# Kernel tuning notes

Hardware: AMD Instinct MI355X
Metric: run time of the kernel (lower is better)

## Reference

```python
import jax, jax.numpy as jnp
import numpy as np

B, S, E, H = 2, 2048, 2048, 16
D = E // H  # head_dim = 128
ROPE_BASE = 10000.0


def _rope_tables(seq_len, dim, dtype):
    inv_freq = 1.0 / (ROPE_BASE ** (jnp.arange(0, dim, 2, dtype=jnp.float32) / dim))
    pos = jnp.arange(seq_len, dtype=jnp.float32)
    freqs = jnp.outer(pos, inv_freq)            # [S, D/2]
    emb = jnp.concatenate([freqs, freqs], -1)    # [S, D]
    return jnp.cos(emb).astype(dtype), jnp.sin(emb).astype(dtype)


def _rotate_half(x):
    x1, x2 = jnp.split(x, 2, axis=-1)
    return jnp.concatenate([-x2, x1], axis=-1)


def _apply_rope(x, cos, sin):
    # x: [B,H,S,D]; cos/sin: [S,D] broadcast over batch+heads
    return x * cos[None, None] + _rotate_half(x) * sin[None, None]


def setup_inputs() -> dict:
    key = jax.random.key(0)
    k1, k2, k3 = jax.random.split(key, 3)
    x = jax.random.normal(k1, (B, S, E), dtype=jnp.float32)
    w_qkv = jax.random.normal(k2, (3 * E, E), dtype=jnp.float32) * (E ** -0.5)
    w_out = jax.random.normal(k3, (E, E), dtype=jnp.float32) * (E ** -0.5)
    return {"x": x, "w_qkv": w_qkv, "w_out": w_out}


def reference(x, w_qkv, w_out):
    b, s, e = x.shape
    qkv = x @ w_qkv.T                                # [B,S,3E]
    q, k, v = jnp.split(qkv, 3, axis=-1)
    def to_heads(t):
        return t.reshape(b, s, H, D).transpose(0, 2, 1, 3)  # [B,H,S,D]
    q, k, v = to_heads(q), to_heads(k), to_heads(v)
    cos, sin = _rope_tables(s, D, x.dtype)
    q = _apply_rope(q, cos, sin)
    k = _apply_rope(k, cos, sin)
    scale = 1.0 / jnp.sqrt(jnp.asarray(D, x.dtype))
    scores = jnp.einsum('bhqd,bhkd->bhqk', q, k) * scale
    causal = jnp.tril(jnp.ones((s, s), dtype=bool))
    scores = jnp.where(causal[None, None], scores, jnp.asarray(-jnp.inf, scores.dtype))
    attn = jax.nn.softmax(scores, axis=-1)
    y = jnp.einsum('bhqk,bhkd->bhqd', attn, v)       # [B,H,S,D]
    y = y.transpose(0, 2, 1, 3).reshape(b, s, e)
    return y @ w_out.T
```

## Files before the change

### kernel.cpp

```cpp
#include <hip/hip_runtime.h>
#include <stdint.h>

constexpr int BATCH = 2;
constexpr int SEQ   = 2048;
constexpr int EMB   = 2048;
constexpr int NH    = 16;
constexpr int HD    = 128;
constexpr int QKV3  = 3 * EMB;

typedef unsigned short u16;
typedef __attribute__((ext_vector_type(8))) short bf16x8;
typedef __attribute__((ext_vector_type(4))) float floatx4;

__device__ inline float bf2f(u16 u) {
  union { unsigned int i; float f; } v; v.i = ((unsigned int)u) << 16; return v.f;
}
__device__ inline u16 f2bf(float f) {
  union { float f; unsigned int i; } v; v.f = f;
  unsigned int x = v.i;
  return (u16)((x + 0x7fffu + ((x >> 16) & 1u)) >> 16);
}

__device__ inline void load_lds16(const void* g, void* l) {
  __builtin_amdgcn_global_load_lds((const __attribute__((address_space(1))) unsigned int*)g,
                                   (__attribute__((address_space(3))) unsigned int*)l,
                                   16, 0, 0);
}

__device__ inline void block_barrier() {
  __builtin_amdgcn_sched_barrier(0);
  asm volatile("" ::: "memory");
  __builtin_amdgcn_s_barrier();
  asm volatile("" ::: "memory");
  __builtin_amdgcn_sched_barrier(0);
}

__global__ void cvt_f32_bf16(const float* __restrict__ src, u16* __restrict__ dst, int n4) {
  const int i = blockIdx.x * blockDim.x + threadIdx.x;
  if (i < n4) {
    const float4 v = ((const float4*)src)[i];
    ushort4 o;
    o.x = f2bf(v.x); o.y = f2bf(v.y); o.z = f2bf(v.z); o.w = f2bf(v.w);
    ((ushort4*)dst)[i] = o;
  }
}

__global__ __launch_bounds__(512, 2) void gemm_bt192(const u16* __restrict__ A,
                                                     const u16* __restrict__ Bm,
                                                     u16* __restrict__ Cb,
                                                     int M, int N, int K) {
  __shared__ __align__(16) u16 sh[57344];
  char* ldsb = (char*)sh;

  const int tid  = threadIdx.x;
  const int wave = tid >> 6, lane = tid & 63;
  const int wrow = wave >> 1;
  const int wcol = wave & 1;
  const int m0 = blockIdx.y * 256, n0 = blockIdx.x * 192;
  const int frow = lane & 15, quad = lane >> 4;
  const int KT = K >> 6;

  const int srow8 = tid >> 3;
  const int scolE = (((tid & 7) ^ (srow8 & 7)) << 3);
  auto stage1 = [&](int t, int d, int j) {
    if (j < 4) {
      const int r = j * 64 + srow8;
      load_lds16(A + (size_t)(m0 + r) * K + t * 64 + scolE,
                 ldsb + d * 57344 + j * 8192 + wave * 1024);
    } else {
      const int bi = j - 4;
      const int r = bi * 64 + srow8;
      load_lds16(Bm + (size_t)(n0 + r) * K + t * 64 + scolE,
                 ldsb + d * 57344 + 32768 + bi * 8192 + wave * 1024);
    }
  };

  floatx4 acc[4][6];
#pragma unroll
  for (int i = 0; i < 4; ++i)
#pragma unroll
    for (int j = 0; j < 6; ++j) acc[i][j] = {0.f, 0.f, 0.f, 0.f};

#pragma unroll
  for (int j = 0; j < 7; ++j) stage1(0, 0, j);

  auto rdA = [&](const char* dbuf, int mi, int kk) -> bf16x8 {
    const int ra = wrow * 64 + mi * 16 + frow;
    const int cb = (kk * 64 + quad * 16) ^ ((ra & 7) << 4);
    return *(const bf16x8*)(dbuf + ra * 128 + cb);
  };
  auto rdB = [&](const char* dbuf, int ni, int kk) -> bf16x8 {
    const int rb = wcol * 96 + ni * 16 + frow;
    const int cb = (kk * 64 + quad * 16) ^ ((rb & 7) << 4);
    return *(const bf16x8*)(dbuf + 32768 + rb * 128 + cb);
  };

  for (int t = 0; t < KT; ++t) {
    const int d = t & 1, dn = d ^ 1;
    const char* dbuf = ldsb + d * 57344;
    const bool pf = (t + 1 < KT);

    asm volatile("s_waitcnt vmcnt(0)" ::: "memory");
    block_barrier();

    bf16x8 a0[2][2], a1[2][2], b0[3][2], b1[3][2];

#pragma unroll
    for (int mi = 0; mi < 2; ++mi)
#pragma unroll
      for (int kk = 0; kk < 2; ++kk) a0[mi][kk] = rdA(dbuf, mi, kk);
#pragma unroll
    for (int ni = 0; ni < 3; ++ni)
#pragma unroll
      for (int kk = 0; kk < 2; ++kk) b0[ni][kk] = rdB(dbuf, ni, kk);
    if (pf) { stage1(t + 1, dn, 0); stage1(t + 1, dn, 1); stage1(t + 1, dn, 2); }
    block_barrier();
    asm volatile("s_waitcnt lgkmcnt(0)" ::: "memory");
    __builtin_amdgcn_sched_barrier(0);
    __builtin_amdgcn_s_setprio(1);
#pragma unroll
    for (int mi = 0; mi < 2; ++mi)
#pragma unroll
      for (int ni = 0; ni < 3; ++ni)
#pragma unroll
        for (int kk = 0; kk < 2; ++kk)
          acc[mi][ni] = __builtin_amdgcn_mfma_f32_16x16x32_bf16(a0[mi][kk], b0[ni][kk], acc[mi][ni], 0, 0, 0);
    __builtin_amdgcn_s_setprio(0);
    block_barrier();

#pragma unroll
    for (int mi = 0; mi < 2; ++mi)
#pragma unroll
      for (int kk = 0; kk < 2; ++kk) a1[mi][kk] = rdA(dbuf, 2 + mi, kk);
    if (pf) { stage1(t + 1, dn, 3); stage1(t + 1, dn, 4); }
    block_barrier();
    asm volatile("s_waitcnt lgkmcnt(0)" ::: "memory");
    __builtin_amdgcn_sched_barrier(0);
    __builtin_amdgcn_s_setprio(1);
#pragma unroll
    for (int mi = 0; mi < 2; ++mi)
#pragma unroll
      for (int ni = 0; ni < 3; ++ni)
#pragma unroll
        for (int kk = 0; kk < 2; ++kk)
          acc[2 + mi][ni] = __builtin_amdgcn_mfma_f32_16x16x32_bf16(a1[mi][kk], b0[ni][kk], acc[2 + mi][ni], 0, 0, 0);
    __builtin_amdgcn_s_setprio(0);
    block_barrier();

#pragma unroll
    for (int ni = 0; ni < 3; ++ni)
#pragma unroll
      for (int kk = 0; kk < 2; ++kk) b1[ni][kk] = rdB(dbuf, 3 + ni, kk);
    if (pf) { stage1(t + 1, dn, 5); stage1(t + 1, dn, 6); }
    block_barrier();
    asm volatile("s_waitcnt lgkmcnt(0)" ::: "memory");
    __builtin_amdgcn_sched_barrier(0);
    __builtin_amdgcn_s_setprio(1);
#pragma unroll
    for (int mi = 0; mi < 2; ++mi)
#pragma unroll
      for (int ni = 0; ni < 3; ++ni)
#pragma unroll
        for (int kk = 0; kk < 2; ++kk)
          acc[2 + mi][3 + ni] = __builtin_amdgcn_mfma_f32_16x16x32_bf16(a1[mi][kk], b1[ni][kk], acc[2 + mi][3 + ni], 0, 0, 0);
    __builtin_amdgcn_s_setprio(0);
    block_barrier();

    __builtin_amdgcn_s_setprio(1);
#pragma unroll
    for (int mi = 0; mi < 2; ++mi)
#pragma unroll
      for (int ni = 0; ni < 3; ++ni)
#pragma unroll
        for (int kk = 0; kk < 2; ++kk)
          acc[mi][3 + ni] = __builtin_amdgcn_mfma_f32_16x16x32_bf16(a0[mi][kk], b1[ni][kk], acc[mi][3 + ni], 0, 0, 0);
    __builtin_amdgcn_s_setprio(0);
    block_barrier();
  }

#pragma unroll
  for (int mi = 0; mi < 4; ++mi)
#pragma unroll
    for (int ni = 0; ni < 6; ++ni) {
      const int row = m0 + wrow * 64 + mi * 16 + quad * 4;
      const int col = n0 + wcol * 96 + ni * 16 + frow;
#pragma unroll
      for (int r = 0; r < 4; ++r)
        Cb[(size_t)(row + r) * N + col] = f2bf(acc[mi][ni][r]);
    }
}

__global__ __launch_bounds__(512, 2) void gemm_bt128f(const u16* __restrict__ A,
                                                      const u16* __restrict__ Bm,
                                                      float* __restrict__ Cf,
                                                      int M, int N, int K) {
  __shared__ __align__(16) u16 sh[49152];
  char* ldsb = (char*)sh;

  const int tid  = threadIdx.x;
  const int wave = tid >> 6, lane = tid & 63;
  const int wrow = wave >> 1;
  const int wcol = wave & 1;
  const int m0 = blockIdx.y * 256, n0 = blockIdx.x * 128;
  const int frow = lane & 15, quad = lane >> 4;
  const int KT = K >> 6;

  const int srow8 = tid >> 3;
  const int scolE = (((tid & 7) ^ (srow8 & 7)) << 3);
  auto stage1 = [&](int t, int d, int j) {
    if (j < 4) {
      const int r = j * 64 + srow8;
      load_lds16(A + (size_t)(m0 + r) * K + t * 64 + scolE,
                 ldsb + d * 49152 + j * 8192 + wave * 1024);
    } else {
      const int bi = j - 4;
      const int r = bi * 64 + srow8;
      load_lds16(Bm + (size_t)(n0 + r) * K + t * 64 + scolE,
                 ldsb + d * 49152 + 32768 + bi * 8192 + wave * 1024);
    }
  };

  floatx4 acc[4][4];
#pragma unroll
  for (int i = 0; i < 4; ++i)
#pragma unroll
    for (int j = 0; j < 4; ++j) acc[i][j] = {0.f, 0.f, 0.f, 0.f};

#pragma unroll
  for (int j = 0; j < 6; ++j) stage1(0, 0, j);

  auto rdA = [&](const char* dbuf, int mi, int kk) -> bf16x8 {
    const int ra = wrow * 64 + mi * 16 + frow;
    const int cb = (kk * 64 + quad * 16) ^ ((ra & 7) << 4);
    return *(const bf16x8*)(dbuf + ra * 128 + cb);
  };
  auto rdB = [&](const char* dbuf, int ni, int kk) -> bf16x8 {
    const int rb = wcol * 64 + ni * 16 + frow;
    const int cb = (kk * 64 + quad * 16) ^ ((rb & 7) << 4);
    return *(const bf16x8*)(dbuf + 32768 + rb * 128 + cb);
  };

  for (int t = 0; t < KT; ++t) {
    const int d = t & 1, dn = d ^ 1;
    const char* dbuf = ldsb + d * 49152;
    const bool pf = (t + 1 < KT);

    asm volatile("s_waitcnt vmcnt(0)" ::: "memory");
    block_barrier();

    bf16x8 af[4][2], b0[2][2], b1[2][2];

#pragma unroll
    for (int mi = 0; mi < 4; ++mi)
#pragma unroll
      for (int kk = 0; kk < 2; ++kk) af[mi][kk] = rdA(dbuf, mi, kk);
#pragma unroll
    for (int ni = 0; ni < 2; ++ni)
#pragma unroll
      for (int kk = 0; kk < 2; ++kk) b0[ni][kk] = rdB(dbuf, ni, kk);
    if (pf) { stage1(t + 1, dn, 0); stage1(t + 1, dn, 1); stage1(t + 1, dn, 2); }
    block_barrier();
    asm volatile("s_waitcnt lgkmcnt(0)" ::: "memory");
    __builtin_amdgcn_sched_barrier(0);
    __builtin_amdgcn_s_setprio(1);
#pragma unroll
    for (int mi = 0; mi < 4; ++mi)
#pragma unroll
      for (int ni = 0; ni < 2; ++ni)
#pragma unroll
        for (int kk = 0; kk < 2; ++kk)
          acc[mi][ni] = __builtin_amdgcn_mfma_f32_16x16x32_bf16(af[mi][kk], b0[ni][kk], acc[mi][ni], 0, 0, 0);
    __builtin_amdgcn_s_setprio(0);
    block_barrier();

#pragma unroll
    for (int ni = 0; ni < 2; ++ni)
#pragma unroll
      for (int kk = 0; kk < 2; ++kk) b1[ni][kk] = rdB(dbuf, 2 + ni, kk);
    if (pf) { stage1(t + 1, dn, 3); stage1(t + 1, dn, 4); stage1(t + 1, dn, 5); }
    block_barrier();
    asm volatile("s_waitcnt lgkmcnt(0)" ::: "memory");
    __builtin_amdgcn_sched_barrier(0);
    __builtin_amdgcn_s_setprio(1);
#pragma unroll
    for (int mi = 0; mi < 4; ++mi)
#pragma unroll
      for (int ni = 0; ni < 2; ++ni)
#pragma unroll
        for (int kk = 0; kk < 2; ++kk)
          acc[mi][2 + ni] = __builtin_amdgcn_mfma_f32_16x16x32_bf16(af[mi][kk], b1[ni][kk], acc[mi][2 + ni], 0, 0, 0);
    __builtin_amdgcn_s_setprio(0);
    block_barrier();
  }

#pragma unroll
  for (int mi = 0; mi < 4; ++mi)
#pragma unroll
    for (int ni = 0; ni < 4; ++ni) {
      const int row = m0 + wrow * 64 + mi * 16 + quad * 4;
      const int col = n0 + wcol * 64 + ni * 16 + frow;
#pragma unroll
      for (int r = 0; r < 4; ++r)
        Cf[(size_t)(row + r) * N + col] = acc[mi][ni][r];
    }
}

__global__ void rope_inplace(u16* __restrict__ qkv) {
  const int t   = blockIdx.x * blockDim.x + threadIdx.x;
  const int j   = t & 63;
  const int idx = t >> 6;
  const int h   = idx & (NH - 1);
  const int bs  = idx >> 4;
  const int s   = bs & (SEQ - 1);

  u16* base = qkv + (size_t)bs * QKV3 + h * HD;

  const float inv_freq = exp2f(-(float)j * (13.287712379549449f / 64.0f));
  const float ang = (float)s * inv_freq;
  const float c = cosf(ang), sn = sinf(ang);

#pragma unroll
  for (int part = 0; part < 2; ++part) {
    u16* p = base + part * EMB;
    const float x1 = bf2f(p[j]), x2 = bf2f(p[j + 64]);
    p[j]      = f2bf(x1 * c - x2 * sn);
    p[j + 64] = f2bf(x2 * c + x1 * sn);
  }
}

__global__ __launch_bounds__(256) void transpose_v(const u16* __restrict__ qkv,
                                                   u16* __restrict__ VT) {
  __shared__ u16 vtile[64][136];
  const int tid = threadIdx.x;
  const int s0 = blockIdx.x * 64;
  const int bh = blockIdx.y;
  const int b = bh >> 4, h = bh & 15;

  const u16* Vp = qkv + (size_t)b * SEQ * QKV3 + 2 * EMB + h * HD;
  {
    const int r = tid >> 2, cp = (tid & 3) * 32;
    const uint4* src = (const uint4*)(Vp + (size_t)(s0 + r) * QKV3 + cp);
    uint4* dst = (uint4*)&vtile[r][cp];
    dst[0] = src[0]; dst[1] = src[1]; dst[2] = src[2]; dst[3] = src[3];
  }
  __syncthreads();
  {
    const int d = tid >> 1, ck = (tid & 1) * 32;
    ushort4 o[8];
#pragma unroll
    for (int i = 0; i < 8; ++i) {
      o[i].x = vtile[ck + i * 4 + 0][d];
      o[i].y = vtile[ck + i * 4 + 1][d];
      o[i].z = vtile[ck + i * 4 + 2][d];
      o[i].w = vtile[ck + i * 4 + 3][d];
    }
    ushort4* dst = (ushort4*)(VT + ((size_t)bh * HD + d) * SEQ + s0 + ck);
#pragma unroll
    for (int i = 0; i < 8; ++i) dst[i] = o[i];
  }
}

constexpr int PSTR = 72;

__global__ __launch_bounds__(256, 2) void attn_mfma(const u16* __restrict__ qkv,
                                                    const u16* __restrict__ VT,
                                                    u16* __restrict__ Y) {
  __shared__ __align__(16) u16 kb[2][64 * 128];
  __shared__ __align__(16) u16 vb[2][64 * 128];
  __shared__ __align__(16) u16 p_sh[4][16][PSTR];

  const int tid  = threadIdx.x;
  const int wave = tid >> 6, lane = tid & 63;
  const int bid  = blockIdx.x;
  const int bh   = bid & 31;
  const int pc   = bid >> 5;
  const int cq   = (pc < 8) ? pc : 23 - pc;
  const int qa   = cq;
  const int qb   = 31 - cq;
  const int b = bh >> 4, h = bh & 15;

  const u16* Qp  = qkv + (size_t)b * SEQ * QKV3 + h * HD;
  const u16* Kp  = Qp + EMB;
  const u16* VTp = VT + (size_t)bh * HD * SEQ;

  const int NT = 32 - cq;

  u16* kbf = &kb[0][0];

  {
    const int rl  = lane >> 4;
    const int cbp = (lane & 15) * 16;
#pragma unroll
    for (int i = 0; i < 8; ++i) {
      const int cc = wave * 8 + i;
      const int r  = cc * 4 + rl;
      const int gq = (r < 64) ? (qa * 64 + r) : (qb * 64 + r - 64);
      const int cbl = cbp ^ ((r & 7) << 4);
      load_lds16(Qp + (size_t)gq * QKV3 + (cbl >> 1), kbf + cc * 512);
    }
  }
  asm volatile("s_waitcnt vmcnt(0)" ::: "memory");
  block_barrier();

  const int frow = lane & 15;
  const int quad = lane >> 4;

  bf16x8 aq[2][4];
#pragma unroll
  for (int m = 0; m < 2; ++m)
#pragma unroll
    for (int ks = 0; ks < 4; ++ks) {
      const int qr = m * 64 + wave * 16 + frow;
      const int cb = (ks * 64 + quad * 16) ^ ((qr & 7) << 4);
      aq[m][ks] = *(const bf16x8*)((const char*)kbf + qr * 256 + cb);
    }
  asm volatile("s_waitcnt lgkmcnt(0)" ::: "memory");
  block_barrier();

  auto stage_k = [&](int t, int sel) {
    const int rl  = lane >> 4;
    const int cbp = (lane & 15) * 16;
#pragma unroll
    for (int i = 0; i < 4; ++i) {
      const int cc = wave * 4 + i;
      const int r  = cc * 4 + rl;
      const int cbl = cbp ^ ((r & 7) << 4);
      load_lds16(Kp + (size_t)(t * 64 + r) * QKV3 + (cbl >> 1), &kb[sel][cc * 512]);
    }
  };
  auto stage_v = [&](int t, int sel) {
    const int rl  = lane >> 3;
    const int cbp = (lane & 7) * 16;
#pragma unroll
    for (int i = 0; i < 4; ++i) {
      const int cc = wave * 4 + i;
      const int r  = cc * 8 + rl;
      const int cbl = cbp ^ ((r & 7) << 4);
      load_lds16(VTp + (size_t)r * SEQ + t * 64 + (cbl >> 1), &vb[sel][cc * 512]);
    }
  };

  floatx4 o_acc[2][8];
#pragma unroll
  for (int m = 0; m < 2; ++m)
#pragma unroll
    for (int dt = 0; dt < 8; ++dt) o_acc[m][dt] = {0.f, 0.f, 0.f, 0.f};
  float l_r[2][4];
#pragma unroll
  for (int m = 0; m < 2; ++m)
#pragma unroll
    for (int r = 0; r < 4; ++r) l_r[m][r] = 0.f;

  const float scale = 0.08838834764831845f;
  const float M0s   = 3.5355339059327378f;

  stage_k(0, 0);
  stage_v(0, 0);

  for (int t = 0; t < NT; ++t) {
    block_barrier();
    const bool havek = (t + 1 < NT);
    if (havek) {
      stage_k(t + 1, (t + 1) & 1);
      stage_v(t + 1, (t + 1) & 1);
      asm volatile("s_waitcnt vmcnt(8)" ::: "memory");
    } else {
      asm volatile("s_waitcnt vmcnt(0)" ::: "memory");
    }
    block_barrier();

    const char* kbuf = (const char*)&kb[t & 1][0];
    const char* vbuf = (const char*)&vb[t & 1][0];
    const bool aAct = (t <= qa);

    floatx4 s4[2][4];
    __builtin_amdgcn_s_setprio(1);
    if (aAct) {
#pragma unroll
      for (int nt = 0; nt < 4; ++nt) {
        floatx4 a0 = {0.f, 0.f, 0.f, 0.f}, a1 = {0.f, 0.f, 0.f, 0.f};
#pragma unroll
        for (int ks = 0; ks < 4; ++ks) {
          const int kr = nt * 16 + frow;
          const int cb = (ks * 64 + quad * 16) ^ ((kr & 7) << 4);
          const bf16x8 bk = *(const bf16x8*)(kbuf + kr * 256 + cb);
          a0 = __builtin_amdgcn_mfma_f32_16x16x32_bf16(aq[0][ks], bk, a0, 0, 0, 0);
          a1 = __builtin_amdgcn_mfma_f32_16x16x32_bf16(aq[1][ks], bk, a1, 0, 0, 0);
        }
        s4[0][nt] = a0; s4[1][nt] = a1;
      }
    } else {
#pragma unroll
      for (int nt = 0; nt < 4; ++nt) {
        floatx4 a1 = {0.f, 0.f, 0.f, 0.f};
#pragma unroll
        for (int ks = 0; ks < 4; ++ks) {
          const int kr = nt * 16 + frow;
          const int cb = (ks * 64 + quad * 16) ^ ((kr & 7) << 4);
          const bf16x8 bk = *(const bf16x8*)(kbuf + kr * 256 + cb);
          a1 = __builtin_amdgcn_mfma_f32_16x16x32_bf16(aq[1][ks], bk, a1, 0, 0, 0);
        }
        s4[1][nt] = a1;
      }
    }
    __builtin_amdgcn_s_setprio(0);

#pragma unroll
    for (int m = 0; m < 2; ++m) {
      if (m == 0 && !aAct) continue;
      const int tdiag = (m == 0) ? qa : qb;
      if (t == tdiag) {
#pragma unroll
        for (int nt = 0; nt < 4; ++nt)
#pragma unroll
          for (int r = 0; r < 4; ++r) {
            const int key = t * 64 + nt * 16 + frow;
            const int qg  = tdiag * 64 + wave * 16 + quad * 4 + r;
            if (key > qg) s4[m][nt][r] = -1.0e30f;
          }
      }
#pragma unroll
      for (int nt = 0; nt < 4; ++nt)
#pragma unroll
        for (int r = 0; r < 4; ++r)
          s4[m][nt][r] = __expf(fmaf(s4[m][nt][r], scale, -M0s));
#pragma unroll
      for (int r = 0; r < 4; ++r)
        l_r[m][r] += (s4[m][0][r] + s4[m][1][r]) + (s4[m][2][r] + s4[m][3][r]);
    }

    __builtin_amdgcn_s_setprio(1);
#pragma unroll
    for (int m = 0; m < 2; ++m) {
      if (m == 0 && !aAct) continue;
#pragma unroll
      for (int nt = 0; nt < 4; ++nt)
#pragma unroll
        for (int r = 0; r < 4; ++r)
          p_sh[wave][quad * 4 + r][nt * 16 + frow] = f2bf(s4[m][nt][r]);
#pragma unroll
      for (int step = 0; step < 2; ++step) {
        const bf16x8 ap = *(const bf16x8*)&p_sh[wave][frow][step * 32 + quad * 8];
#pragma unroll
        for (int dt = 0; dt < 8; ++dt) {
          const int vr = dt * 16 + frow;
          const int cb = (step * 64 + quad * 16) ^ ((vr & 7) << 4);
          const bf16x8 bv = *(const bf16x8*)(vbuf + vr * 128 + cb);
          o_acc[m][dt] = __builtin_amdgcn_mfma_f32_16x16x32_bf16(ap, bv, o_acc[m][dt], 0, 0, 0);
        }
      }
    }
    __builtin_amdgcn_s_setprio(0);
  }

#pragma unroll
  for (int off = 1; off <= 8; off <<= 1)
#pragma unroll
    for (int m = 0; m < 2; ++m)
#pragma unroll
      for (int r = 0; r < 4; ++r) l_r[m][r] += __shfl_xor(l_r[m][r], off);

#pragma unroll
  for (int m = 0; m < 2; ++m) {
    const int qbase = ((m == 0) ? qa : qb) * 64 + wave * 16;
    float invl[4];
#pragma unroll
    for (int r = 0; r < 4; ++r) invl[r] = 1.f / l_r[m][r];
#pragma unroll
    for (int dt = 0; dt < 8; ++dt)
#pragma unroll
      for (int r = 0; r < 4; ++r) {
        const int qg = qbase + quad * 4 + r;
        const size_t off = ((size_t)b * SEQ + qg) * EMB + h * HD + dt * 16 + frow;
        Y[off] = f2bf(o_acc[m][dt][r] * invl[r]);
      }
  }
}

extern "C" void kernel_launch(void* const* d_in, const int* in_sizes, int n_in,
                              void* d_out, int out_size, void* d_ws, size_t ws_size,
                              hipStream_t stream) {
  const float* x_f     = (const float*)d_in[0];
  const float* w_qkv_f = (const float*)d_in[1];
  const float* w_out_f = (const float*)d_in[2];
  float* out = (float*)d_out;

  const int M = BATCH * SEQ;
  const size_t n_x    = (size_t)M * EMB;
  const size_t n_wqkv = (size_t)3 * EMB * EMB;
  const size_t n_wout = (size_t)EMB * EMB;

  u16* xb    = (u16*)d_ws;
  u16* wqkvb = xb + n_x;
  u16* qkv   = wqkvb + n_wqkv;
  u16* VT    = qkv + (size_t)M * QKV3;
  u16* woutb = wqkvb;
  u16* Yb    = xb;

  cvt_f32_bf16<<<(int)((n_x / 4 + 255) / 256), 256, 0, stream>>>(x_f, xb, (int)(n_x / 4));
  cvt_f32_bf16<<<(int)((n_wqkv / 4 + 255) / 256), 256, 0, stream>>>(w_qkv_f, wqkvb, (int)(n_wqkv / 4));

  gemm_bt192<<<dim3(QKV3 / 192, M / 256), 512, 0, stream>>>(
      xb, wqkvb, qkv, M, QKV3, EMB);

  rope_inplace<<<(BATCH * SEQ * NH * 64) / 256, 256, 0, stream>>>(qkv);
  transpose_v<<<dim3(SEQ / 64, BATCH * NH), 256, 0, stream>>>(qkv, VT);

  cvt_f32_bf16<<<(int)((n_wout / 4 + 255) / 256), 256, 0, stream>>>(w_out_f, woutb, (int)(n_wout / 4));

  attn_mfma<<<dim3((SEQ / 128) * BATCH * NH), 256, 0, stream>>>(qkv, VT, Yb);

  gemm_bt128f<<<dim3(EMB / 128, M / 256), 512, 0, stream>>>(
      Yb, woutb, out, M, EMB, EMB);
}
```

Before: 357.2 us.

## Issue full-tile prefetch at iteration start and drop intra-loop barriers in GEMMs

Both bf16 GEMM kernels, the QKV projection and the output projection, are changed the same way. Each now issues all async global-to-LDS loads for the next K tile in one batch right after the top-of-loop barrier. Previously those loads were split into three or two chunks, each wrapped in its own barrier pair. The per-phase block barriers, lgkmcnt waits and the trailing barrier are removed, leaving one barrier per K iteration. The aim is to cut synchronization stalls and let LDS reads overlap MFMA work, at the cost of less finely interleaved memory traffic and more reliance on the compiler's scheduling of LDS reads.

```diff
diff --git a/kernel.cpp b/kernel.cpp
--- a/kernel.cpp
+++ b/kernel.cpp
@@ -62,13 +62,15 @@
 
   const int srow8 = tid >> 3;
   const int scolE = (((tid & 7) ^ (srow8 & 7)) << 3);
-  auto stage1 = [&](int t, int d, int j) {
-    if (j < 4) {
-      const int r = j * 64 + srow8;
+  auto stageT = [&](int t, int d) {
+#pragma unroll
+    for (int a = 0; a < 4; ++a) {
+      const int r = a * 64 + srow8;
       load_lds16(A + (size_t)(m0 + r) * K + t * 64 + scolE,
-                 ldsb + d * 57344 + j * 8192 + wave * 1024);
-    } else {
-      const int bi = j - 4;
+                 ldsb + d * 57344 + a * 8192 + wave * 1024);
+    }
+#pragma unroll
+    for (int bi = 0; bi < 3; ++bi) {
       const int r = bi * 64 + srow8;
       load_lds16(Bm + (size_t)(n0 + r) * K + t * 64 + scolE,
                  ldsb + d * 57344 + 32768 + bi * 8192 + wave * 1024);
@@ -81,8 +83,7 @@
 #pragma unroll
     for (int j = 0; j < 6; ++j) acc[i][j] = {0.f, 0.f, 0.f, 0.f};
 
-#pragma unroll
-  for (int j = 0; j < 7; ++j) stage1(0, 0, j);
+  stageT(0, 0);
 
   auto rdA = [&](const char* dbuf, int mi, int kk) -> bf16x8 {
     const int ra = wrow * 64 + mi * 16 + frow;
@@ -98,13 +99,14 @@
   for (int t = 0; t < KT; ++t) {
     const int d = t & 1, dn = d ^ 1;
     const char* dbuf = ldsb + d * 57344;
-    const bool pf = (t + 1 < KT);
 
     asm volatile("s_waitcnt vmcnt(0)" ::: "memory");
     block_barrier();
 
+    if (t + 1 < KT) stageT(t + 1, dn);
+    __builtin_amdgcn_sched_barrier(0);
+
     bf16x8 a0[2][2], a1[2][2], b0[3][2], b1[3][2];
-
 #pragma unroll
     for (int mi = 0; mi < 2; ++mi)
 #pragma unroll
@@ -113,10 +115,11 @@
     for (int ni = 0; ni < 3; ++ni)
 #pragma unroll
       for (int kk = 0; kk < 2; ++kk) b0[ni][kk] = rdB(dbuf, ni, kk);
-    if (pf) { stage1(t + 1, dn, 0); stage1(t + 1, dn, 1); stage1(t + 1, dn, 2); }
-    block_barrier();
-    asm volatile("s_waitcnt lgkmcnt(0)" ::: "memory");
-    __builtin_amdgcn_sched_barrier(0);
+#pragma unroll
+    for (int mi = 0; mi < 2; ++mi)
+#pragma unroll
+      for (int kk = 0; kk < 2; ++kk) a1[mi][kk] = rdA(dbuf, 2 + mi, kk);
+
     __builtin_amdgcn_s_setprio(1);
 #pragma unroll
     for (int mi = 0; mi < 2; ++mi)
@@ -126,16 +129,12 @@
         for (int kk = 0; kk < 2; ++kk)
           acc[mi][ni] = __builtin_amdgcn_mfma_f32_16x16x32_bf16(a0[mi][kk], b0[ni][kk], acc[mi][ni], 0, 0, 0);
     __builtin_amdgcn_s_setprio(0);
-    block_barrier();
-
-#pragma unroll
-    for (int mi = 0; mi < 2; ++mi)
-#pragma unroll
-      for (int kk = 0; kk < 2; ++kk) a1[mi][kk] = rdA(dbuf, 2 + mi, kk);
-    if (pf) { stage1(t + 1, dn, 3); stage1(t + 1, dn, 4); }
-    block_barrier();
-    asm volatile("s_waitcnt lgkmcnt(0)" ::: "memory");
-    __builtin_amdgcn_sched_barrier(0);
+
+#pragma unroll
+    for (int ni = 0; ni < 3; ++ni)
+#pragma unroll
+      for (int kk = 0; kk < 2; ++kk) b1[ni][kk] = rdB(dbuf, 3 + ni, kk);
+
     __builtin_amdgcn_s_setprio(1);
 #pragma unroll
     for (int mi = 0; mi < 2; ++mi)
@@ -144,18 +143,6 @@
 #pragma unroll
         for (int kk = 0; kk < 2; ++kk)
           acc[2 + mi][ni] = __builtin_amdgcn_mfma_f32_16x16x32_bf16(a1[mi][kk], b0[ni][kk], acc[2 + mi][ni], 0, 0, 0);
-    __builtin_amdgcn_s_setprio(0);
-    block_barrier();
-
-#pragma unroll
-    for (int ni = 0; ni < 3; ++ni)
-#pragma unroll
-      for (int kk = 0; kk < 2; ++kk) b1[ni][kk] = rdB(dbuf, 3 + ni, kk);
-    if (pf) { stage1(t + 1, dn, 5); stage1(t + 1, dn, 6); }
-    block_barrier();
-    asm volatile("s_waitcnt lgkmcnt(0)" ::: "memory");
-    __builtin_amdgcn_sched_barrier(0);
-    __builtin_amdgcn_s_setprio(1);
 #pragma unroll
     for (int mi = 0; mi < 2; ++mi)
 #pragma unroll
@@ -163,10 +150,6 @@
 #pragma unroll
         for (int kk = 0; kk < 2; ++kk)
           acc[2 + mi][3 + ni] = __builtin_amdgcn_mfma_f32_16x16x32_bf16(a1[mi][kk], b1[ni][kk], acc[2 + mi][3 + ni], 0, 0, 0);
-    __builtin_amdgcn_s_setprio(0);
-    block_barrier();
-
-    __builtin_amdgcn_s_setprio(1);
 #pragma unroll
     for (int mi = 0; mi < 2; ++mi)
 #pragma unroll
@@ -175,7 +158,6 @@
         for (int kk = 0; kk < 2; ++kk)
           acc[mi][3 + ni] = __builtin_amdgcn_mfma_f32_16x16x32_bf16(a0[mi][kk], b1[ni][kk], acc[mi][3 + ni], 0, 0, 0);
     __builtin_amdgcn_s_setprio(0);
-    block_barrier();
   }
 
 #pragma unroll
@@ -207,13 +189,15 @@
 
   const int srow8 = tid >> 3;
   const int scolE = (((tid & 7) ^ (srow8 & 7)) << 3);
-  auto stage1 = [&](int t, int d, int j) {
-    if (j < 4) {
-      const int r = j * 64 + srow8;
+  auto stageT = [&](int t, int d) {
+#pragma unroll
+    for (int a = 0; a < 4; ++a) {
+      const int r = a * 64 + srow8;
       load_lds16(A + (size_t)(m0 + r) * K + t * 64 + scolE,
-                 ldsb + d * 49152 + j * 8192 + wave * 1024);
-    } else {
-      const int bi = j - 4;
+                 ldsb + d * 49152 + a * 8192 + wave * 1024);
+    }
+#pragma unroll
+    for (int bi = 0; bi < 2; ++bi) {
       const int r = bi * 64 + srow8;
       load_lds16(Bm + (size_t)(n0 + r) * K + t * 64 + scolE,
                  ldsb + d * 49152 + 32768 + bi * 8192 + wave * 1024);
@@ -226,8 +210,7 @@
 #pragma unroll
     for (int j = 0; j < 4; ++j) acc[i][j] = {0.f, 0.f, 0.f, 0.f};
 
-#pragma unroll
-  for (int j = 0; j < 6; ++j) stage1(0, 0, j);
+  stageT(0, 0);
 
   auto rdA = [&](const char* dbuf, int mi, int kk) -> bf16x8 {
     const int ra = wrow * 64 + mi * 16 + frow;
@@ -243,13 +226,14 @@
   for (int t = 0; t < KT; ++t) {
     const int d = t & 1, dn = d ^ 1;
     const char* dbuf = ldsb + d * 49152;
-    const bool pf = (t + 1 < KT);
 
     asm volatile("s_waitcnt vmcnt(0)" ::: "memory");
     block_barrier();
 
+    if (t + 1 < KT) stageT(t + 1, dn);
+    __builtin_amdgcn_sched_barrier(0);
+
     bf16x8 af[4][2], b0[2][2], b1[2][2];
-
 #pragma unroll
     for (int mi = 0; mi < 4; ++mi)
 #pragma unroll
@@ -258,10 +242,7 @@
     for (int ni = 0; ni < 2; ++ni)
 #pragma unroll
       for (int kk = 0; kk < 2; ++kk) b0[ni][kk] = rdB(dbuf, ni, kk);
-    if (pf) { stage1(t + 1, dn, 0); stage1(t + 1, dn, 1); stage1(t + 1, dn, 2); }
-    block_barrier();
-    asm volatile("s_waitcnt lgkmcnt(0)" ::: "memory");
-    __builtin_amdgcn_sched_barrier(0);
+
     __builtin_amdgcn_s_setprio(1);
 #pragma unroll
     for (int mi = 0; mi < 4; ++mi)
@@ -271,16 +252,12 @@
         for (int kk = 0; kk < 2; ++kk)
           acc[mi][ni] = __builtin_amdgcn_mfma_f32_16x16x32_bf16(af[mi][kk], b0[ni][kk], acc[mi][ni], 0, 0, 0);
     __builtin_amdgcn_s_setprio(0);
-    block_barrier();
 
 #pragma unroll
     for (int ni = 0; ni < 2; ++ni)
 #pragma unroll
       for (int kk = 0; kk < 2; ++kk) b1[ni][kk] = rdB(dbuf, 2 + ni, kk);
-    if (pf) { stage1(t + 1, dn, 3); stage1(t + 1, dn, 4); stage1(t + 1, dn, 5); }
-    block_barrier();
-    asm volatile("s_waitcnt lgkmcnt(0)" ::: "memory");
-    __builtin_amdgcn_sched_barrier(0);
+
     __builtin_amdgcn_s_setprio(1);
 #pragma unroll
     for (int mi = 0; mi < 4; ++mi)
@@ -290,7 +267,6 @@
         for (int kk = 0; kk < 2; ++kk)
           acc[mi][2 + ni] = __builtin_amdgcn_mfma_f32_16x16x32_bf16(af[mi][kk], b1[ni][kk], acc[mi][2 + ni], 0, 0, 0);
     __builtin_amdgcn_s_setprio(0);
-    block_barrier();
   }
 
 #pragma unroll
```

Result: no change. 356.4 us (-0.2%).
